# Performance work log

Hardware: AMD Instinct MI355X
Metric: run time of the kernel (lower is better)

Reference implementation:

```python
import jax, jax.numpy as jnp
import numpy as np

BATCH = 512          # bs_large + bs_small
COMBINED_BS = 320    # bs_large + bs_small // (r_large // r_small)
R = 64               # r_large
K = 4096             # hidden dim, fixed in the TIR kernel
N_ADAPT = 80         # combined adapters


def setup_inputs() -> dict:
    key = jax.random.key(0)
    k1, k2, k3, k4 = jax.random.split(key, 4)
    x = jax.random.normal(k1, (BATCH, 1, K), dtype=jnp.float32)
    xids = jax.random.randint(k2, (COMBINED_BS * R,), 0, BATCH, dtype=jnp.int32)
    wids = jax.random.randint(k3, (COMBINED_BS,), 0, N_ADAPT, dtype=jnp.int32)
    A = jax.random.normal(k4, (N_ADAPT, K, R), dtype=jnp.float32) * 0.02
    return {"x": x, "xids": xids, "wids": wids, "A": A}


def reference(x, xids, wids, A):
    # out[c, 0, r] = sum_k x[xids[c*R + r], 0, k] * A[wids[c], k, r]
    C = wids.shape[0]
    r = A.shape[2]
    tok = xids.reshape(C, r)          # per-output-element token ids
    xg = x[tok, 0, :]                 # (C, R, K) gathered activations
    Ag = A[wids]                      # (C, K, R) gathered adapters
    out = jnp.einsum('crk,ckr->cr', xg, Ag)
    return out[:, None, :]            # (C, 1, R)
```

## Files before the change

kernel.cpp:

```cpp
#include <hip/hip_runtime.h>
#include <stdint.h>

namespace {
constexpr int BATCH  = 512;
constexpr int CBS    = 320;
constexpr int R      = 64;
constexpr int K      = 4096;
constexpr int NADAPT = 80;
constexpr int GRP    = 4;
constexpr int NGMAX  = 140;
constexpr int SPLIT  = 16;
constexpr int KS     = K / SPLIT;
constexpr int TK     = 32;
constexpr int NTILE  = KS / TK;
constexpr int NT     = 256;

constexpr size_t WS_GRP_OFF = 64;
constexpr size_t WS_X_OFF   = 4096;
constexpr size_t WS_NEEDED  = WS_X_OFF + (size_t)BATCH * K * 2;

__device__ inline uint16_t f2bf(float f) {
    uint32_t u = __float_as_uint(f);
    u += 0x7fffu + ((u >> 16) & 1u);
    return (uint16_t)(u >> 16);
}
__device__ inline float bflo(uint32_t u) { return __uint_as_float(u << 16); }
__device__ inline float bfhi(uint32_t u) { return __uint_as_float(u & 0xffff0000u); }

__device__ __forceinline__ void dot8(float& acc, const uint4 v, const float (&a)[8]) {
    acc = fmaf(bflo(v.x), a[0], acc);
    acc = fmaf(bfhi(v.x), a[1], acc);
    acc = fmaf(bflo(v.y), a[2], acc);
    acc = fmaf(bfhi(v.y), a[3], acc);
    acc = fmaf(bflo(v.z), a[4], acc);
    acc = fmaf(bfhi(v.z), a[5], acc);
    acc = fmaf(bflo(v.w), a[6], acc);
    acc = fmaf(bfhi(v.w), a[7], acc);
}

#define WAITL() asm volatile("s_waitcnt lgkmcnt(0)" ::: "memory")
#define SCHED0() __builtin_amdgcn_sched_barrier(0)
#define SBAR()  __builtin_amdgcn_s_barrier()

template<int T, bool IX2, bool IA1, bool WRT, int WN>
__device__ __forceinline__ void body(
    uint32_t* __restrict__ xs_base,
    const uint16_t* __restrict__ xrow,
    const float* __restrict__ Ab,
    int wv, int r,
    uint4 (&pxN)[4], const uint4 (&pxW)[4],
    float (&aN)[8], const float (&aC)[8],
    float& acc0, float& acc1, float& acc2, float& acc3)
{
    const uint32_t* Bp = xs_base + (T & 1) * 4096 + wv * 256 + 4 * r;
    const uint4 xv0 = *(const uint4*)(Bp + 0 * 1024);
    const uint4 xv1 = *(const uint4*)(Bp + 1 * 1024);
    const uint4 xv2 = *(const uint4*)(Bp + 2 * 1024);
    const uint4 xv3 = *(const uint4*)(Bp + 3 * 1024);
    if constexpr (IX2) {
        const uint4* s2 = (const uint4*)(xrow + (T + 2) * TK);
        pxN[0] = s2[0]; pxN[1] = s2[1]; pxN[2] = s2[2]; pxN[3] = s2[3];
    }
    if constexpr (IA1) {
#pragma unroll
        for (int q = 0; q < 8; ++q)
            aN[q] = Ab[((size_t)((T + 1) * TK) + wv * 8 + q) * R];
    }
    asm volatile("s_waitcnt vmcnt(%0)" :: "i"(WN) : "memory");
    WAITL();
    SCHED0();
    dot8(acc0, xv0, aC);
    dot8(acc1, xv1, aC);
    dot8(acc2, xv2, aC);
    dot8(acc3, xv3, aC);
    if constexpr (WRT) {
        uint32_t* wb = xs_base + ((T + 1) & 1) * 4096 + wv * 1024 + 4 * r;
        *(uint4*)(wb +   0) = pxW[0];
        *(uint4*)(wb + 256) = pxW[1];
        *(uint4*)(wb + 512) = pxW[2];
        *(uint4*)(wb + 768) = pxW[3];
        WAITL(); SCHED0();
        SBAR();
        SCHED0();
    }
}
}

__global__ __launch_bounds__(256)
void prep(const float* __restrict__ x, uint16_t* __restrict__ xb,
          const int* __restrict__ wids, int* __restrict__ hdr,
          int* __restrict__ grp, float* __restrict__ out, int out_size)
{
    const int bid = blockIdx.x;
    const int t   = threadIdx.x;
    if (bid == 0) {
        __shared__ int hist[NADAPT];
        __shared__ int offs[NADAPT];
        __shared__ int gbase[NADAPT + 1];
        __shared__ int sperm[CBS];
        if (t < NADAPT) hist[t] = 0;
        __syncthreads();
        for (int c = t; c < CBS; c += 256) atomicAdd(&hist[wids[c]], 1);
        __syncthreads();
        if (t == 0) {
            int run = 0, grun = 0;
            for (int i = 0; i < NADAPT; ++i) {
                offs[i]  = run;  run  += hist[i];
                gbase[i] = grun; grun += (hist[i] + GRP - 1) / GRP;
            }
            gbase[NADAPT] = grun;
            hdr[0] = grun;
        }
        __syncthreads();
        for (int c = t; c < CBS; c += 256) {
            const int pos = atomicAdd(&offs[wids[c]], 1);
            sperm[pos] = c;
        }
        __syncthreads();
        for (int w = t; w < NADAPT; w += 256) {
            const int cnt   = hist[w];
            const int start = offs[w] - cnt;
            const int gb    = gbase[w];
            for (int i = 0; i < cnt; i += GRP) {
                const int gi = gb + i / GRP;
#pragma unroll
                for (int j = 0; j < GRP; ++j)
                    grp[GRP * gi + j] = (i + j < cnt) ? sperm[start + i + j] : -1;
            }
        }
    } else if (bid <= BATCH * K / 1024) {
        const int i = (bid - 1) * 256 + t;
        const float4 v = ((const float4*)x)[i];
        ushort4 o;
        o.x = f2bf(v.x); o.y = f2bf(v.y); o.z = f2bf(v.z); o.w = f2bf(v.w);
        ((ushort4*)xb)[i] = o;
    } else {
        const int i4 = (bid - (1 + BATCH * K / 1024)) * 256 + t;
        const int e  = i4 * 4;
        if (e + 3 < out_size) {
            ((float4*)out)[i4] = make_float4(0.f, 0.f, 0.f, 0.f);
        } else {
            for (int q = e; q < out_size; ++q) out[q] = 0.f;
        }
    }
}

__global__ __launch_bounds__(NT, 4)
void lora_main(const int* __restrict__ xids,
               const int* __restrict__ wids,
               const float* __restrict__ A,
               const uint16_t* __restrict__ xb,
               const int* __restrict__ hdr,
               const int* __restrict__ grp,
               float* __restrict__ out)
{
    __shared__ __align__(16) uint32_t xs[2][GRP * 1024];
    __shared__ float red[4 * GRP * 64];

    const int bid = blockIdx.x;
    const int g   = bid >> 4;
    const int s   = bid & 15;
    if (g >= hdr[0]) return;

    const int t  = threadIdx.x;
    const int wv = t >> 6;
    const int r  = t & 63;

    const int* gp = grp + GRP * g;
    const int gc0 = gp[0], gc1 = gp[1], gc2 = gp[2], gc3 = gp[3];
    const int myc_raw = (wv == 0) ? gc0 : (wv == 1) ? gc1 : (wv == 2) ? gc2 : gc3;
    const int myc = (myc_raw >= 0) ? myc_raw : gc0;
    const int wid = wids[gc0];

    const uint16_t* __restrict__ xrow = xb + (size_t)xids[myc * R + r] * K + s * KS;
    const float* __restrict__ Ab = A + (size_t)wid * (K * R) + (size_t)(s * KS) * R + r;

    float acc0 = 0.f, acc1 = 0.f, acc2 = 0.f, acc3 = 0.f;
    uint4 pxA[4], pxB[4];
    float aA[8], aB[8];

    {
        const uint4* s0p = (const uint4*)xrow;
        pxA[0] = s0p[0]; pxA[1] = s0p[1]; pxA[2] = s0p[2]; pxA[3] = s0p[3];
        SCHED0();
        const uint4* s1p = (const uint4*)(xrow + TK);
        pxB[0] = s1p[0]; pxB[1] = s1p[1]; pxB[2] = s1p[2]; pxB[3] = s1p[3];
        SCHED0();
#pragma unroll
        for (int q = 0; q < 8; ++q) aA[q] = Ab[(size_t)(wv * 8 + q) * R];
        asm volatile("s_waitcnt vmcnt(12)" ::: "memory");
        uint32_t* wb = &xs[0][wv * 1024 + 4 * r];
        *(uint4*)(wb +   0) = pxA[0];
        *(uint4*)(wb + 256) = pxA[1];
        *(uint4*)(wb + 512) = pxA[2];
        *(uint4*)(wb + 768) = pxA[3];
        WAITL(); SCHED0();
        SBAR();
        SCHED0();
    }

    uint32_t* xsb = &xs[0][0];
    body<0, true,  true,  true, 12>(xsb, xrow, Ab, wv, r, pxA, pxB, aB, aA, acc0, acc1, acc2, acc3);
    body<1, true,  true,  true, 12>(xsb, xrow, Ab, wv, r, pxB, pxA, aA, aB, acc0, acc1, acc2, acc3);
    body<2, true,  true,  true, 12>(xsb, xrow, Ab, wv, r, pxA, pxB, aB, aA, acc0, acc1, acc2, acc3);
    body<3, true,  true,  true, 12>(xsb, xrow, Ab, wv, r, pxB, pxA, aA, aB, acc0, acc1, acc2, acc3);
    body<4, true,  true,  true, 12>(xsb, xrow, Ab, wv, r, pxA, pxB, aB, aA, acc0, acc1, acc2, acc3);
    body<5, true,  true,  true, 12>(xsb, xrow, Ab, wv, r, pxB, pxA, aA, aB, acc0, acc1, acc2, acc3);
    body<6, false, true,  true,  8>(xsb, xrow, Ab, wv, r, pxA, pxB, aB, aA, acc0, acc1, acc2, acc3);
    body<7, false, false, false, 0>(xsb, xrow, Ab, wv, r, pxB, pxA, aA, aB, acc0, acc1, acc2, acc3);

    red[wv * 256 +   0 + r] = acc0;
    red[wv * 256 +  64 + r] = acc1;
    red[wv * 256 + 128 + r] = acc2;
    red[wv * 256 + 192 + r] = acc3;
    __syncthreads();
    const float sum = red[0 * 256 + wv * 64 + r] + red[1 * 256 + wv * 64 + r] +
                      red[2 * 256 + wv * 64 + r] + red[3 * 256 + wv * 64 + r];
    if (myc_raw >= 0)
        atomicAdd(&out[myc_raw * R + r], sum);
}

__global__ __launch_bounds__(NT)
void lora_fallback(const float* __restrict__ x,
                   const int*   __restrict__ xids,
                   const int*   __restrict__ wids,
                   const float* __restrict__ A,
                   float*       __restrict__ out)
{
    constexpr int FKS = 512, FTK = 64, FNT_TILES = 8, FNW = 4;
    __shared__ float xsf[FTK * R];
    __shared__ float red[FNW * R];
    const int bid  = blockIdx.x;
    const int c    = bid >> 3;
    const int s    = bid & 7;
    const int t    = threadIdx.x;
    const int wave = t >> 6;
    const int lane = t & 63;
    const int r4   = lane & 15;
    const int kq   = lane >> 4;
    const int wid  = wids[c];
    const float* __restrict__ Aw = A + (size_t)wid * (K * R);
    const int rw  = t >> 2;
    const int jq  = t & 3;
    const int tok = xids[c * R + rw];
    const float* __restrict__ xrow = x + (size_t)tok * K + s * FKS + jq * 16;
    float4 acc = make_float4(0.f, 0.f, 0.f, 0.f);
    float4 pv[4];
    {
        const float4* src = (const float4*)xrow;
#pragma unroll
        for (int ii = 0; ii < 4; ++ii) pv[ii] = src[ii];
    }
    for (int tile = 0; tile < FNT_TILES; ++tile) {
#pragma unroll
        for (int ii = 0; ii < 4; ++ii) {
            const int kk = jq * 16 + ii * 4;
            xsf[(kk + 0) * R + rw] = pv[ii].x;
            xsf[(kk + 1) * R + rw] = pv[ii].y;
            xsf[(kk + 2) * R + rw] = pv[ii].z;
            xsf[(kk + 3) * R + rw] = pv[ii].w;
        }
        __syncthreads();
        if (tile + 1 < FNT_TILES) {
            const float4* src = (const float4*)(xrow + (tile + 1) * FTK);
#pragma unroll
            for (int ii = 0; ii < 4; ++ii) pv[ii] = src[ii];
        }
        const int kw = wave * 16 + kq;
        const float* __restrict__ Ap =
            Aw + (size_t)(s * FKS + tile * FTK + kw) * R + 4 * r4;
#pragma unroll
        for (int i = 0; i < 4; ++i) {
            float4 av = *(const float4*)(Ap + (size_t)(4 * i) * R);
            float4 xv = *(const float4*)(&xsf[(kw + 4 * i) * R + 4 * r4]);
            acc.x = fmaf(xv.x, av.x, acc.x);
            acc.y = fmaf(xv.y, av.y, acc.y);
            acc.z = fmaf(xv.z, av.z, acc.z);
            acc.w = fmaf(xv.w, av.w, acc.w);
        }
        __syncthreads();
    }
#pragma unroll
    for (int m = 16; m < 64; m <<= 1) {
        acc.x += __shfl_xor(acc.x, m, 64);
        acc.y += __shfl_xor(acc.y, m, 64);
        acc.z += __shfl_xor(acc.z, m, 64);
        acc.w += __shfl_xor(acc.w, m, 64);
    }
    if (kq == 0) {
        float* rd = &red[wave * R + 4 * r4];
        rd[0] = acc.x; rd[1] = acc.y; rd[2] = acc.z; rd[3] = acc.w;
    }
    __syncthreads();
    if (wave == 0) {
        float sum = red[lane] + red[R + lane] + red[2 * R + lane] + red[3 * R + lane];
        atomicAdd(&out[c * R + lane], sum);
    }
}

extern "C" void kernel_launch(void* const* d_in, const int* in_sizes, int n_in,
                              void* d_out, int out_size, void* d_ws, size_t ws_size,
                              hipStream_t stream)
{
    (void)in_sizes; (void)n_in;
    const float* x    = (const float*)d_in[0];
    const int*   xids = (const int*)d_in[1];
    const int*   wids = (const int*)d_in[2];
    const float* A    = (const float*)d_in[3];
    float* out        = (float*)d_out;

    if (ws_size >= WS_NEEDED) {
        int*      hdr = (int*)d_ws;
        int*      grp = (int*)((char*)d_ws + WS_GRP_OFF);
        uint16_t* xbw = (uint16_t*)((char*)d_ws + WS_X_OFF);
        const int ncvt = BATCH * K / 1024;
        const int nz   = (out_size + 1023) / 1024;
        hipLaunchKernelGGL(prep, dim3(1 + ncvt + nz), dim3(256), 0, stream,
                           x, xbw, wids, hdr, grp, out, out_size);
        hipLaunchKernelGGL(lora_main, dim3(NGMAX * SPLIT), dim3(NT), 0, stream,
                           xids, wids, A, xbw, hdr, grp, out);
    } else {
        hipMemsetAsync(out, 0, (size_t)out_size * sizeof(float), stream);
        hipLaunchKernelGGL(lora_fallback, dim3(CBS * 8), dim3(NT), 0, stream,
                           x, xids, wids, A, out);
    }
}
```

Before: 158.1 us.

## Halve K-split, coalesce x row loads across lanes, and swizzle LDS layout

Cuts the K-split from 16 to 8, so each block covers twice the K range with 16 pipelined tiles instead of 8, which halves the number of blocks and the atomic adds. The global x loads are remapped so four adjacent lanes read one token row's 64-byte tile segment, making the loads more coalesced. An XOR swizzle is added to the shared-memory write and read indices to avoid bank conflicts. The trade-off is fewer blocks (less parallelism across CUs) and a longer serial loop per block.

Result: slower. 225.0 us (+42.3%).

```diff
diff --git a/kernel.cpp b/kernel.cpp
--- a/kernel.cpp
+++ b/kernel.cpp
@@ -9,7 +9,7 @@
 constexpr int NADAPT = 80;
 constexpr int GRP    = 4;
 constexpr int NGMAX  = 140;
-constexpr int SPLIT  = 16;
+constexpr int SPLIT  = 8;
 constexpr int KS     = K / SPLIT;
 constexpr int TK     = 32;
 constexpr int NTILE  = KS / TK;
@@ -44,22 +44,23 @@
 
 template<int T, bool IX2, bool IA1, bool WRT, int WN>
 __device__ __forceinline__ void body(
-    uint32_t* __restrict__ xs_base,
-    const uint16_t* __restrict__ xrow,
+    uint4* __restrict__ xsb,
+    const uint16_t* const (&xp)[4],
     const float* __restrict__ Ab,
-    int wv, int r,
+    int wv, int rdi, int swi,
     uint4 (&pxN)[4], const uint4 (&pxW)[4],
     float (&aN)[8], const float (&aC)[8],
     float& acc0, float& acc1, float& acc2, float& acc3)
 {
-    const uint32_t* Bp = xs_base + (T & 1) * 4096 + wv * 256 + 4 * r;
-    const uint4 xv0 = *(const uint4*)(Bp + 0 * 1024);
-    const uint4 xv1 = *(const uint4*)(Bp + 1 * 1024);
-    const uint4 xv2 = *(const uint4*)(Bp + 2 * 1024);
-    const uint4 xv3 = *(const uint4*)(Bp + 3 * 1024);
+    const uint4* Bp = xsb + (T & 1) * 1024 + rdi;
+    const uint4 xv0 = Bp[0];
+    const uint4 xv1 = Bp[256];
+    const uint4 xv2 = Bp[512];
+    const uint4 xv3 = Bp[768];
     if constexpr (IX2) {
-        const uint4* s2 = (const uint4*)(xrow + (T + 2) * TK);
-        pxN[0] = s2[0]; pxN[1] = s2[1]; pxN[2] = s2[2]; pxN[3] = s2[3];
+#pragma unroll
+        for (int i = 0; i < 4; ++i)
+            pxN[i] = *(const uint4*)(xp[i] + (T + 2) * TK);
     }
     if constexpr (IA1) {
 #pragma unroll
@@ -74,11 +75,10 @@
     dot8(acc2, xv2, aC);
     dot8(acc3, xv3, aC);
     if constexpr (WRT) {
-        uint32_t* wb = xs_base + ((T + 1) & 1) * 4096 + wv * 1024 + 4 * r;
-        *(uint4*)(wb +   0) = pxW[0];
-        *(uint4*)(wb + 256) = pxW[1];
-        *(uint4*)(wb + 512) = pxW[2];
-        *(uint4*)(wb + 768) = pxW[3];
+        uint4* wb = xsb + ((T + 1) & 1) * 1024 + swi;
+#pragma unroll
+        for (int i = 0; i < 4; ++i)
+            wb[64 * i] = pxW[i];
         WAITL(); SCHED0();
         SBAR();
         SCHED0();
@@ -154,12 +154,12 @@
                const int* __restrict__ grp,
                float* __restrict__ out)
 {
-    __shared__ __align__(16) uint32_t xs[2][GRP * 1024];
+    __shared__ __align__(16) uint4 xs[2][1024];
     __shared__ float red[4 * GRP * 64];
 
     const int bid = blockIdx.x;
-    const int g   = bid >> 4;
-    const int s   = bid & 15;
+    const int g   = bid >> 3;
+    const int s   = bid & 7;
     if (g >= hdr[0]) return;
 
     const int t  = threadIdx.x;
@@ -172,42 +172,57 @@
     const int myc = (myc_raw >= 0) ? myc_raw : gc0;
     const int wid = wids[gc0];
 
-    const uint16_t* __restrict__ xrow = xb + (size_t)xids[myc * R + r] * K + s * KS;
-    const float* __restrict__ Ab = A + (size_t)wid * (K * R) + (size_t)(s * KS) * R + r;
+    const uint16_t* xp[4];
+#pragma unroll
+    for (int i = 0; i < 4; ++i)
+        xp[i] = xb + (size_t)xids[myc * R + 16 * i + (r >> 2)] * K
+                   + s * KS + (r & 3) * 8;
+
+    const int rdi = r * 4 + (wv ^ ((r >> 1) & 3));
+    const int swi = wv * 256 + (r >> 2) * 4 + ((r & 3) ^ ((r >> 3) & 3));
+
+    const float* __restrict__ Ab =
+        A + (size_t)wid * (K * R) + (size_t)(s * KS) * R + r;
 
     float acc0 = 0.f, acc1 = 0.f, acc2 = 0.f, acc3 = 0.f;
     uint4 pxA[4], pxB[4];
     float aA[8], aB[8];
 
     {
-        const uint4* s0p = (const uint4*)xrow;
-        pxA[0] = s0p[0]; pxA[1] = s0p[1]; pxA[2] = s0p[2]; pxA[3] = s0p[3];
+#pragma unroll
+        for (int i = 0; i < 4; ++i) pxA[i] = *(const uint4*)(xp[i]);
         SCHED0();
-        const uint4* s1p = (const uint4*)(xrow + TK);
-        pxB[0] = s1p[0]; pxB[1] = s1p[1]; pxB[2] = s1p[2]; pxB[3] = s1p[3];
+#pragma unroll
+        for (int i = 0; i < 4; ++i) pxB[i] = *(const uint4*)(xp[i] + TK);
         SCHED0();
 #pragma unroll
         for (int q = 0; q < 8; ++q) aA[q] = Ab[(size_t)(wv * 8 + q) * R];
         asm volatile("s_waitcnt vmcnt(12)" ::: "memory");
-        uint32_t* wb = &xs[0][wv * 1024 + 4 * r];
-        *(uint4*)(wb +   0) = pxA[0];
-        *(uint4*)(wb + 256) = pxA[1];
-        *(uint4*)(wb + 512) = pxA[2];
-        *(uint4*)(wb + 768) = pxA[3];
+        uint4* wb = &xs[0][0] + swi;
+#pragma unroll
+        for (int i = 0; i < 4; ++i) wb[64 * i] = pxA[i];
         WAITL(); SCHED0();
         SBAR();
         SCHED0();
     }
 
-    uint32_t* xsb = &xs[0][0];
-    body<0, true,  true,  true, 12>(xsb, xrow, Ab, wv, r, pxA, pxB, aB, aA, acc0, acc1, acc2, acc3);
-    body<1, true,  true,  true, 12>(xsb, xrow, Ab, wv, r, pxB, pxA, aA, aB, acc0, acc1, acc2, acc3);
-    body<2, true,  true,  true, 12>(xsb, xrow, Ab, wv, r, pxA, pxB, aB, aA, acc0, acc1, acc2, acc3);
-    body<3, true,  true,  true, 12>(xsb, xrow, Ab, wv, r, pxB, pxA, aA, aB, acc0, acc1, acc2, acc3);
-    body<4, true,  true,  true, 12>(xsb, xrow, Ab, wv, r, pxA, pxB, aB, aA, acc0, acc1, acc2, acc3);
-    body<5, true,  true,  true, 12>(xsb, xrow, Ab, wv, r, pxB, pxA, aA, aB, acc0, acc1, acc2, acc3);
-    body<6, false, true,  true,  8>(xsb, xrow, Ab, wv, r, pxA, pxB, aB, aA, acc0, acc1, acc2, acc3);
-    body<7, false, false, false, 0>(xsb, xrow, Ab, wv, r, pxB, pxA, aA, aB, acc0, acc1, acc2, acc3);
+    uint4* xsb = &xs[0][0];
+    body< 0, true,  true,  true, 12>(xsb, xp, Ab, wv, rdi, swi, pxA, pxB, aB, aA, acc0, acc1, acc2, acc3);
+    body< 1, true,  true,  true, 12>(xsb, xp, Ab, wv, rdi, swi, pxB, pxA, aA, aB, acc0, acc1, acc2, acc3);
+    body< 2, true,  true,  true, 12>(xsb, xp, Ab, wv, rdi, swi, pxA, pxB, aB, aA, acc0, acc1, acc2, acc3);
+    body< 3, true,  true,  true, 12>(xsb, xp, Ab, wv, rdi, swi, pxB, pxA, aA, aB, acc0, acc1, acc2, acc3);
+    body< 4, true,  true,  true, 12>(xsb, xp, Ab, wv, rdi, swi, pxA, pxB, aB, aA, acc0, acc1, acc2, acc3);
+    body< 5, true,  true,  true, 12>(xsb, xp, Ab, wv, rdi, swi, pxB, pxA, aA, aB, acc0, acc1, acc2, acc3);
+    body< 6, true,  true,  true, 12>(xsb, xp, Ab, wv, rdi, swi, pxA, pxB, aB, aA, acc0, acc1, acc2, acc3);
+    body< 7, true,  true,  true, 12>(xsb, xp, Ab, wv, rdi, swi, pxB, pxA, aA, aB, acc0, acc1, acc2, acc3);
+    body< 8, true,  true,  true, 12>(xsb, xp, Ab, wv, rdi, swi, pxA, pxB, aB, aA, acc0, acc1, acc2, acc3);
+    body< 9, true,  true,  true, 12>(xsb, xp, Ab, wv, rdi, swi, pxB, pxA, aA, aB, acc0, acc1, acc2, acc3);
+    body<10, true,  true,  true, 12>(xsb, xp, Ab, wv, rdi, swi, pxA, pxB, aB, aA, acc0, acc1, acc2, acc3);
+    body<11, true,  true,  true, 12>(xsb, xp, Ab, wv, rdi, swi, pxB, pxA, aA, aB, acc0, acc1, acc2, acc3);
+    body<12, true,  true,  true, 12>(xsb, xp, Ab, wv, rdi, swi, pxA, pxB, aB, aA, acc0, acc1, acc2, acc3);
+    body<13, true,  true,  true, 12>(xsb, xp, Ab, wv, rdi, swi, pxB, pxA, aA, aB, acc0, acc1, acc2, acc3);
+    body<14, false, true,  true,  8>(xsb, xp, Ab, wv, rdi, swi, pxA, pxB, aB, aA, acc0, acc1, acc2, acc3);
+    body<15, false, false, false, 0>(xsb, xp, Ab, wv, rdi, swi, pxB, pxA, aA, aB, acc0, acc1, acc2, acc3);
 
     red[wv * 256 +   0 + r] = acc0;
     red[wv * 256 +  64 + r] = acc1;
```
